# Optimization experiments

Measured on AMD Instinct MI355X. Metric: run time of the kernel, lower is better.

The kernel has to match this reference:

```python
import jax, jax.numpy as jnp
import numpy as np

B, T, D_MODEL, N_HEADS, N_KV = 2, 2048, 1024, 16, 4
HEAD = D_MODEL // N_HEADS  # 64
NEG_INF = -1e9


def sine_table(features, length):
    # standard RoPE frequency table: theta_i = 10000^(2i/d)
    fraction = jnp.arange(0, features, 2, dtype=jnp.float32) / features
    timescale = 10000.0 ** fraction  # (features/2,)
    sinusoid = jnp.arange(length, dtype=jnp.float32)[:, None] / timescale[None, :]
    sinusoid = jnp.concatenate([sinusoid, sinusoid], axis=-1)  # (L, features)
    return jnp.sin(sinusoid), jnp.cos(sinusoid)


def rotate_half(x):
    x1, x2 = jnp.split(x, 2, axis=-1)
    return jnp.concatenate([-x2, x1], axis=-1)


def apply_rope(x, sin, cos):
    # x: (B, H, T, D); sin/cos: (L, D)
    t = x.shape[-2]
    return x * cos[:t][None, None] + rotate_half(x) * sin[:t][None, None]


def setup_inputs() -> dict:
    key = jax.random.key(0)
    k1, k2, k3, k4 = jax.random.split(key, 4)
    return {
        'q': jax.random.normal(k1, (B, T, D_MODEL), dtype=jnp.float32),
        'k': jax.random.normal(k2, (B, T, N_KV * HEAD), dtype=jnp.float32),
        'v': jax.random.normal(k3, (B, T, N_KV * HEAD), dtype=jnp.float32),
        'w_out': jax.random.normal(k4, (D_MODEL, D_MODEL), dtype=jnp.float32) * 0.02,
    }


def reference(q, k, v, w_out):
    Bq, Tq, C = q.shape
    head = C // N_HEADS
    # split heads: q -> (B, n_heads, T, head); k/v -> (B, n_kv, T, head)
    qh = q.reshape(Bq, Tq, N_HEADS, head).transpose(0, 2, 1, 3)
    kh = k.reshape(Bq, Tq, N_KV, head).transpose(0, 2, 1, 3)
    vh = v.reshape(Bq, Tq, N_KV, head).transpose(0, 2, 1, 3)
    # inline RoPE on q and k
    sin, cos = sine_table(head, Tq)
    qh = apply_rope(qh, sin, cos)
    kh = apply_rope(kh, sin, cos)
    # GQA repeat of kv heads to match q heads
    rep = N_HEADS // N_KV
    kh = jnp.repeat(kh, rep, axis=1)
    vh = jnp.repeat(vh, rep, axis=1)
    # manual scaled-dot-product attention with causal masking (full T^2 logits)
    logits = jnp.einsum('bhqd,bhkd->bhqk', qh, kh) / jnp.sqrt(jnp.float32(head))
    causal = jnp.tril(jnp.ones((Tq, Tq), dtype=jnp.float32))
    logits = jnp.where(causal == 0, NEG_INF, logits)
    attn = jax.nn.softmax(logits, axis=-1)
    out = jnp.einsum('bhqk,bhkd->bhqd', attn, vh)
    out = out.transpose(0, 2, 1, 3).reshape(Bq, Tq, C)
    return out @ w_out
```

## Files before the change

### kernel.cpp

```cpp
#include <hip/hip_runtime.h>
#include <math.h>

#define T_SEQ 2048
#define NH    16
#define NKV   4

typedef __attribute__((ext_vector_type(8)))  _Float16 f16x8;
typedef __attribute__((ext_vector_type(4)))  _Float16 f16x4;
typedef __attribute__((ext_vector_type(2)))  __fp16   fp16x2b;
typedef __attribute__((ext_vector_type(4)))  float    f32x4;

#if __has_builtin(__builtin_amdgcn_exp2f)
#define EXP2F(x) __builtin_amdgcn_exp2f(x)
#else
#define EXP2F(x) exp2f(x)
#endif

#define QSCALE 0.18033688011112042f

#define LDS_BARRIER()                                        \
    do {                                                     \
        __builtin_amdgcn_sched_barrier(0);                   \
        asm volatile("s_waitcnt lgkmcnt(0)" ::: "memory");   \
        __builtin_amdgcn_s_barrier();                        \
        __builtin_amdgcn_sched_barrier(0);                   \
    } while (0)

__global__ __launch_bounds__(256) void prep_kernel(const float* __restrict__ k,
                                                   const float* __restrict__ v,
                                                   const float* __restrict__ w,
                                                   float2* __restrict__ tb,
                                                   _Float16* __restrict__ Kr,
                                                   _Float16* __restrict__ Vt,
                                                   _Float16* __restrict__ Wt)
{
    __shared__ _Float16 L[64 * 72];
    const int bx = blockIdx.x;
    if (bx < 256) {
        int idx = bx * 256 + threadIdx.x;
        int i = idx & 31, t = idx >> 5;
        float inv = __expf((float)i * (-9.210340371976184f / 32.0f));
        float ang = (float)t * inv;
        tb[idx] = make_float2(cosf(ang), sinf(ang));
    } else if (bx < 512) {
        int idx = (bx - 256) * 256 + threadIdx.x;
        int i   = idx & 31;
        int t   = idx >> 5;
        float inv = __expf((float)i * (-9.210340371976184f / 32.0f));
        float ang = (float)t * inv;
        float sn = sinf(ang), cs = cosf(ang);
        #pragma unroll
        for (int bk = 0; bk < 8; ++bk) {
            const float* src = k + ((size_t)(bk >> 2) * T_SEQ + t) * 256 + (bk & 3) * 64 + i;
            float x1 = src[0], x2 = src[32];
            _Float16* dst = Kr + ((size_t)bk * T_SEQ + t) * 64 + i;
            dst[0]  = (_Float16)(x1 * cs - x2 * sn);
            dst[32] = (_Float16)(x2 * cs + x1 * sn);
        }
    } else if (bx < 768) {
        const int id = bx - 512;
        const int t0 = (id & 31) * 64, bk = id >> 5;
        const int b = bk >> 2, kh = bk & 3;
        const int rr = threadIdx.x >> 2, pp = threadIdx.x & 3;
        const float* src = v + ((size_t)(b * T_SEQ + t0 + rr)) * 256 + kh * 64 + pp * 16;
        f32x4 s0 = *(const f32x4*)(src), s1 = *(const f32x4*)(src + 4);
        f32x4 s2 = *(const f32x4*)(src + 8), s3 = *(const f32x4*)(src + 12);
        _Float16* lp = &L[rr * 72 + pp * 16];
        #pragma unroll
        for (int j = 0; j < 4; ++j) { lp[j] = (_Float16)s0[j]; lp[4+j] = (_Float16)s1[j];
                                      lp[8+j] = (_Float16)s2[j]; lp[12+j] = (_Float16)s3[j]; }
        __syncthreads();
        f16x8 w0, w1;
        #pragma unroll
        for (int j = 0; j < 8; ++j) w0[j] = L[(pp * 16 + j) * 72 + rr];
        #pragma unroll
        for (int j = 0; j < 8; ++j) w1[j] = L[(pp * 16 + 8 + j) * 72 + rr];
        _Float16* dst = Vt + ((size_t)bk * 64 + rr) * T_SEQ + t0 + pp * 16;
        *(f16x8*)dst = w0; *(f16x8*)(dst + 8) = w1;
    } else {
        const int id = bx - 768;
        const int k0 = (id & 15) * 64, n0 = (id >> 4) * 64;
        const int rr = threadIdx.x >> 2, pp = threadIdx.x & 3;
        const float* src = w + (size_t)(k0 + rr) * 1024 + n0 + pp * 16;
        f32x4 s0 = *(const f32x4*)(src), s1 = *(const f32x4*)(src + 4);
        f32x4 s2 = *(const f32x4*)(src + 8), s3 = *(const f32x4*)(src + 12);
        _Float16* lp = &L[rr * 72 + pp * 16];
        #pragma unroll
        for (int j = 0; j < 4; ++j) { lp[j] = (_Float16)s0[j]; lp[4+j] = (_Float16)s1[j];
                                      lp[8+j] = (_Float16)s2[j]; lp[12+j] = (_Float16)s3[j]; }
        __syncthreads();
        f16x8 w0, w1;
        #pragma unroll
        for (int j = 0; j < 8; ++j) w0[j] = L[(pp * 16 + j) * 72 + rr];
        #pragma unroll
        for (int j = 0; j < 8; ++j) w1[j] = L[(pp * 16 + 8 + j) * 72 + rr];
        _Float16* dst = Wt + (size_t)(n0 + rr) * 1024 + k0 + pp * 16;
        *(f16x8*)dst = w0; *(f16x8*)(dst + 8) = w1;
    }
}


__global__ __launch_bounds__(256) void attn_kernel(const float* __restrict__ q,
                                                   const float2* __restrict__ tb,
                                                   const _Float16* __restrict__ Kr,
                                                   const _Float16* __restrict__ Vt,
                                                   _Float16* __restrict__ AO)
{
    __shared__ _Float16 smem[16384];

    const int wid  = threadIdx.x >> 6;
    const int lane = threadIdx.x & 63;
    const int bh = blockIdx.x & 31;
    const int pp = blockIdx.x >> 5;
    const int p  = (pp < 8) ? pp : (23 - pp);
    const int qb0 = p, qb1 = 31 - p;
    const int b = bh >> 4, h = bh & 15;
    const int kh = h >> 2;
    const int bkh = b * NKV + kh;
    const int g = lane >> 4, r = lane & 15;

    const int srow   = wid * 16 + (lane >> 3);
    const int schunk = lane & 7;
    const _Float16* kgbase = Kr + (size_t)bkh * T_SEQ * 64;
    const _Float16* vgbase = Vt + (size_t)bkh * 64 * T_SEQ;
    const int kd0 = srow * 64 + ((schunk ^ (srow & 7)) * 8);
    const int kd1 = kd0 + 8 * 64;

    f16x8 stK0, stK1, stV0, stV1;
    {
        const _Float16* kg = kgbase + (size_t)srow * 64 + schunk * 8;
        stK0 = *(const f16x8*)(kg);
        stK1 = *(const f16x8*)(kg + 8 * 64);
        const _Float16* vg = vgbase + (size_t)srow * T_SEQ + schunk * 8;
        stV0 = *(const f16x8*)(vg);
        stV1 = *(const f16x8*)(vg + 8 * T_SEQ);
    }

    f16x8 qa[2][2];
    #pragma unroll
    for (int tl = 0; tl < 2; ++tl) {
        const int t = (tl ? qb1 : qb0) * 64 + wid * 16 + r;
        const float* qs = q + ((size_t)b * T_SEQ + t) * 1024 + h * 64 + 8 * g;
        const float2* tp = tb + t * 32 + 8 * g;
        #pragma unroll
        for (int j = 0; j < 8; ++j) {
            float x0 = qs[j], x1 = qs[32 + j];
            float2 cs = tp[j];
            qa[tl][0][j] = (_Float16)((x0 * cs.x - x1 * cs.y) * QSCALE);
            qa[tl][1][j] = (_Float16)((x1 * cs.x + x0 * cs.y) * QSCALE);
        }
    }

    *(f16x8*)(&smem[kd0])        = stK0;
    *(f16x8*)(&smem[kd1])        = stK1;
    *(f16x8*)(&smem[8192 + kd0]) = stV0;
    *(f16x8*)(&smem[8192 + kd1]) = stV1;
    __syncthreads();

    f32x4 o[2][4];
    f32x4 o4[2];
    #pragma unroll
    for (int tl = 0; tl < 2; ++tl) {
        #pragma unroll
        for (int db = 0; db < 4; ++db) o[tl][db] = (f32x4){0.f,0.f,0.f,0.f};
        o4[tl] = (f32x4){0.f,0.f,0.f,0.f};
    }
    const f16x4 onesf = {(_Float16)1.f, (_Float16)1.f, (_Float16)1.f, (_Float16)1.f};
    float mrun[2] = {-INFINITY, -INFINITY};
    int cur = 0;

    for (int kvb = 0; kvb <= qb1; ++kvb) {
        const bool hasNext = (kvb < qb1);
        if (hasNext) {
            const int nb = (kvb + 1) * 64;
            const _Float16* kg = kgbase + (size_t)(nb + srow) * 64 + schunk * 8;
            stK0 = *(const f16x8*)(kg);
            stK1 = *(const f16x8*)(kg + 8 * 64);
            const _Float16* vg = vgbase + (size_t)srow * T_SEQ + nb + schunk * 8;
            stV0 = *(const f16x8*)(vg);
            stV1 = *(const f16x8*)(vg + 8 * T_SEQ);
        }
        const bool act0 = (kvb <= qb0);
        const _Float16* ks = smem + cur * 4096;
        const _Float16* vs = smem + 8192 + cur * 4096;

        f32x4 stt[2][4];
        __builtin_amdgcn_s_setprio(1);
        #pragma unroll
        for (int kt = 0; kt < 4; ++kt) {
            f16x8 ka0 = *(const f16x8*)(ks + (kt*16 + r) * 64 + ((g       ^ (r & 7)) * 8));
            f16x8 ka1 = *(const f16x8*)(ks + (kt*16 + r) * 64 + (((4 + g) ^ (r & 7)) * 8));
            f32x4 s1 = {0.f,0.f,0.f,0.f};
            s1 = __builtin_amdgcn_mfma_f32_16x16x32_f16(ka0, qa[1][0], s1, 0, 0, 0);
            s1 = __builtin_amdgcn_mfma_f32_16x16x32_f16(ka1, qa[1][1], s1, 0, 0, 0);
            stt[1][kt] = s1;
            if (act0) {
                f32x4 s0 = {0.f,0.f,0.f,0.f};
                s0 = __builtin_amdgcn_mfma_f32_16x16x32_f16(ka0, qa[0][0], s0, 0, 0, 0);
                s0 = __builtin_amdgcn_mfma_f32_16x16x32_f16(ka1, qa[0][1], s0, 0, 0, 0);
                stt[0][kt] = s0;
            }
        }
        __builtin_amdgcn_s_setprio(0);

        if (kvb == qb0) {
            #pragma unroll
            for (int kt = 0; kt < 4; ++kt)
                #pragma unroll
                for (int j = 0; j < 4; ++j)
                    if (kt*16 + 4*g + j > wid*16 + r) stt[0][kt][j] = -1e9f;
        }
        if (kvb == qb1) {
            #pragma unroll
            for (int kt = 0; kt < 4; ++kt)
                #pragma unroll
                for (int j = 0; j < 4; ++j)
                    if (kt*16 + 4*g + j > wid*16 + r) stt[1][kt][j] = -1e9f;
        }

        f16x4 pf[2][4];
        #pragma unroll
        for (int tl = 0; tl < 2; ++tl) {
            if (tl == 0 && !act0) continue;
            float a0 = fmaxf(fmaxf(stt[tl][0][0], stt[tl][0][1]),
                             fmaxf(stt[tl][0][2], stt[tl][0][3]));
            float a1 = fmaxf(fmaxf(stt[tl][1][0], stt[tl][1][1]),
                             fmaxf(stt[tl][1][2], stt[tl][1][3]));
            float a2 = fmaxf(fmaxf(stt[tl][2][0], stt[tl][2][1]),
                             fmaxf(stt[tl][2][2], stt[tl][2][3]));
            float a3 = fmaxf(fmaxf(stt[tl][3][0], stt[tl][3][1]),
                             fmaxf(stt[tl][3][2], stt[tl][3][3]));
            float pmL = fmaxf(fmaxf(a0, a1), fmaxf(a2, a3));
            if (!__all(pmL <= mrun[tl] + 8.0f)) {
                float pm = fmaxf(pmL, __shfl_xor(pmL, 16));
                pm = fmaxf(pm, __shfl_xor(pm, 32));
                float mn   = fmaxf(mrun[tl], pm);
                float corr = EXP2F(mrun[tl] - mn);
                mrun[tl]   = mn;
                f32x4 cf = { __shfl(corr, 4*g + 0), __shfl(corr, 4*g + 1),
                             __shfl(corr, 4*g + 2), __shfl(corr, 4*g + 3) };
                o[tl][0] *= cf; o[tl][1] *= cf; o[tl][2] *= cf; o[tl][3] *= cf;
                o4[tl]   *= cf;
            }
            #pragma unroll
            for (int kt = 0; kt < 4; ++kt) {
                float p0 = EXP2F(stt[tl][kt][0] - mrun[tl]);
                float p1 = EXP2F(stt[tl][kt][1] - mrun[tl]);
                float p2 = EXP2F(stt[tl][kt][2] - mrun[tl]);
                float p3 = EXP2F(stt[tl][kt][3] - mrun[tl]);
                union { unsigned u[2]; f16x4 v; } pk;
                union { fp16x2b hh; unsigned u; } c0, c1;
                c0.hh = __builtin_amdgcn_cvt_pkrtz(p0, p1);
                c1.hh = __builtin_amdgcn_cvt_pkrtz(p2, p3);
                pk.u[0] = c0.u; pk.u[1] = c1.u;
                pf[tl][kt] = pk.v;
            }
        }

        __builtin_amdgcn_s_setprio(1);
        #pragma unroll
        for (int kt = 0; kt < 4; ++kt) {
            const int vc = ((2*kt + (g >> 1)) ^ (r & 7)) * 8 + (g & 1) * 4;
            f16x4 v0 = *(const f16x4*)(vs + (0*16 + r) * 64 + vc);
            f16x4 v1 = *(const f16x4*)(vs + (1*16 + r) * 64 + vc);
            f16x4 v2 = *(const f16x4*)(vs + (2*16 + r) * 64 + vc);
            f16x4 v3 = *(const f16x4*)(vs + (3*16 + r) * 64 + vc);
            o[1][0] = __builtin_amdgcn_mfma_f32_16x16x16f16(pf[1][kt], v0, o[1][0], 0, 0, 0);
            o[1][1] = __builtin_amdgcn_mfma_f32_16x16x16f16(pf[1][kt], v1, o[1][1], 0, 0, 0);
            o[1][2] = __builtin_amdgcn_mfma_f32_16x16x16f16(pf[1][kt], v2, o[1][2], 0, 0, 0);
            o[1][3] = __builtin_amdgcn_mfma_f32_16x16x16f16(pf[1][kt], v3, o[1][3], 0, 0, 0);
            o4[1]   = __builtin_amdgcn_mfma_f32_16x16x16f16(pf[1][kt], onesf, o4[1], 0, 0, 0);
            if (act0) {
                o[0][0] = __builtin_amdgcn_mfma_f32_16x16x16f16(pf[0][kt], v0, o[0][0], 0, 0, 0);
                o[0][1] = __builtin_amdgcn_mfma_f32_16x16x16f16(pf[0][kt], v1, o[0][1], 0, 0, 0);
                o[0][2] = __builtin_amdgcn_mfma_f32_16x16x16f16(pf[0][kt], v2, o[0][2], 0, 0, 0);
                o[0][3] = __builtin_amdgcn_mfma_f32_16x16x16f16(pf[0][kt], v3, o[0][3], 0, 0, 0);
                o4[0]   = __builtin_amdgcn_mfma_f32_16x16x16f16(pf[0][kt], onesf, o4[0], 0, 0, 0);
            }
        }
        __builtin_amdgcn_s_setprio(0);

        if (hasNext) {
            _Float16* kw = smem + (cur ^ 1) * 4096;
            _Float16* vw = smem + 8192 + (cur ^ 1) * 4096;
            *(f16x8*)(&kw[kd0]) = stK0;
            *(f16x8*)(&kw[kd1]) = stK1;
            *(f16x8*)(&vw[kd0]) = stV0;
            *(f16x8*)(&vw[kd1]) = stV1;
            cur ^= 1;
        }
        __syncthreads();
    }

    #pragma unroll
    for (int tl = 0; tl < 2; ++tl) {
        f32x4 li;
        #pragma unroll
        for (int j = 0; j < 4; ++j) li[j] = 1.0f / o4[tl][j];
        _Float16* Os = smem + tl * 4608;
        #pragma unroll
        for (int db = 0; db < 4; ++db) {
            f32x4 ov = o[tl][db] * li;
            #pragma unroll
            for (int j = 0; j < 4; ++j)
                Os[(wid*16 + 4*g + j) * 72 + db*16 + r] = (_Float16)ov[j];
        }
    }
    __syncthreads();
    {
        const int row = threadIdx.x >> 2, part = threadIdx.x & 3;
        #pragma unroll
        for (int tl = 0; tl < 2; ++tl) {
            const int qb = tl ? qb1 : qb0;
            const _Float16* src = smem + tl * 4608 + row * 72 + part * 16;
            _Float16* dst = AO + ((size_t)b * T_SEQ + qb * 64 + row) * 1024 + h * 64 + part * 16;
            *(f16x8*)dst       = *(const f16x8*)src;
            *(f16x8*)(dst + 8) = *(const f16x8*)(src + 8);
        }
    }
}


#define AST 40
__global__ __launch_bounds__(256) void gemm_kernel(const _Float16* __restrict__ A,
                                                   const _Float16* __restrict__ Bt,
                                                   float* __restrict__ C)
{
    __shared__ _Float16 As[2][128 * AST];
    __shared__ _Float16 Bs[2][64 * AST];
    const int tid  = threadIdx.x;
    const int by   = blockIdx.x & 31;
    const int bx   = blockIdx.x >> 5;
    const int lane = tid & 63;
    const int wid  = tid >> 6;
    const int g = lane >> 4, r = lane & 15;
    const int wm = wid >> 1, wn = wid & 1;

    f32x4 acc[4][2];
    #pragma unroll
    for (int i = 0; i < 4; ++i)
        #pragma unroll
        for (int j = 0; j < 2; ++j) acc[i][j] = (f32x4){0.f,0.f,0.f,0.f};

    const int c0 = tid, c1 = tid + 256;
    const size_t a0off = (size_t)(by*128 + (c0 >> 2)) * 1024 + (c0 & 3) * 8;
    const size_t a1off = (size_t)(by*128 + (c1 >> 2)) * 1024 + (c1 & 3) * 8;
    const size_t b0off = (size_t)(bx*64  + (c0 >> 2)) * 1024 + (c0 & 3) * 8;
    const int ad0 = (c0 >> 2) * AST + (c0 & 3) * 8;
    const int ad1 = (c1 >> 2) * AST + (c1 & 3) * 8;

    f16x8 pA0 = *(const f16x8*)(A  + a0off);
    f16x8 pA1 = *(const f16x8*)(A  + a1off);
    f16x8 pB0 = *(const f16x8*)(Bt + b0off);
    *(f16x8*)(&As[0][ad0]) = pA0;
    *(f16x8*)(&As[0][ad1]) = pA1;
    *(f16x8*)(&Bs[0][ad0]) = pB0;
    f16x8 sA0B = *(const f16x8*)(A  + a0off + 32);
    f16x8 sA1B = *(const f16x8*)(A  + a1off + 32);
    f16x8 sB0B = *(const f16x8*)(Bt + b0off + 32);
    f16x8 sA0A, sA1A, sB0A;
    __syncthreads();

    auto iter_body = [&](int kt,
                         f16x8& iA0, f16x8& iA1, f16x8& iB0,
                         f16x8& oA0, f16x8& oA1, f16x8& oB0) {
        if (kt + 2 < 32) {
            iA0 = *(const f16x8*)(A  + a0off + (kt + 2) * 32);
            iA1 = *(const f16x8*)(A  + a1off + (kt + 2) * 32);
            iB0 = *(const f16x8*)(Bt + b0off + (kt + 2) * 32);
        }
        const int cur = kt & 1;
        f16x8 af[4], bfv[2];
        #pragma unroll
        for (int mi = 0; mi < 4; ++mi)
            af[mi] = *(const f16x8*)(&As[cur][(wm*64 + mi*16 + r) * AST + 8 * g]);
        #pragma unroll
        for (int ni = 0; ni < 2; ++ni)
            bfv[ni] = *(const f16x8*)(&Bs[cur][(wn*32 + ni*16 + r) * AST + 8 * g]);
        __builtin_amdgcn_s_setprio(1);
        #pragma unroll
        for (int mi = 0; mi < 4; ++mi)
            #pragma unroll
            for (int ni = 0; ni < 2; ++ni)
                acc[mi][ni] = __builtin_amdgcn_mfma_f32_16x16x32_f16(
                                  af[mi], bfv[ni], acc[mi][ni], 0, 0, 0);
        __builtin_amdgcn_s_setprio(0);
        if (kt + 1 < 32) {
            *(f16x8*)(&As[cur ^ 1][ad0]) = oA0;
            *(f16x8*)(&As[cur ^ 1][ad1]) = oA1;
            *(f16x8*)(&Bs[cur ^ 1][ad0]) = oB0;
        }
        LDS_BARRIER();
    };

    #pragma unroll 2
    for (int kt = 0; kt < 32; kt += 2) {
        iter_body(kt,     sA0A, sA1A, sB0A, sA0B, sA1B, sB0B);
        iter_body(kt + 1, sA0B, sA1B, sB0B, sA0A, sA1A, sB0A);
    }

    #pragma unroll
    for (int mi = 0; mi < 4; ++mi)
        #pragma unroll
        for (int ni = 0; ni < 2; ++ni)
            #pragma unroll
            for (int j = 0; j < 4; ++j)
                C[(size_t)(by*128 + wm*64 + mi*16 + 4*g + j) * 1024
                  + bx*64 + wn*32 + ni*16 + r] = acc[mi][ni][j];
}


extern "C" void kernel_launch(void* const* d_in, const int* in_sizes, int n_in,
                              void* d_out, int out_size, void* d_ws, size_t ws_size,
                              hipStream_t stream) {
    const float* q = (const float*)d_in[0];
    const float* k = (const float*)d_in[1];
    const float* v = (const float*)d_in[2];
    const float* w = (const float*)d_in[3];
    float* out = (float*)d_out;

    char* ws = (char*)d_ws;
    float2*   tb = (float2*)(ws);
    _Float16* Kr = (_Float16*)(ws + ((size_t)1 << 20));
    _Float16* Vt = (_Float16*)(ws + ((size_t)3 << 20));
    _Float16* Wt = (_Float16*)(ws + ((size_t)5 << 20));
    _Float16* AO = (_Float16*)(ws + ((size_t)7 << 20));

    hipLaunchKernelGGL(prep_kernel,  dim3(1024), dim3(256), 0, stream, k, v, w, tb, Kr, Vt, Wt);
    hipLaunchKernelGGL(attn_kernel,  dim3(512),  dim3(256), 0, stream, q, tb, Kr, Vt, AO);
    hipLaunchKernelGGL(gemm_kernel,  dim3(512),  dim3(256), 0, stream, AO, Wt, out);
}
```

Baseline: 72.59 us.

## Split attention KV range across two blocks and merge partial results

Each (batch, head, query-pair) attention work item is split into two halves over the KV range, doubling the grid to 1024 blocks. Each half stores its fp16 partial output plus per-row running max and denominator. A new merge kernel rescales and combines the two partials. The aim is better occupancy and load balance across the MI355X CUs. The cost is an extra kernel launch, extra global traffic for partial outputs, and another fp16 rounding step.

```diff
diff --git a/kernel.cpp b/kernel.cpp
--- a/kernel.cpp
+++ b/kernel.cpp
@@ -100,20 +100,28 @@
 }
 
 
-__global__ __launch_bounds__(256) void attn_kernel(const float* __restrict__ q,
-                                                   const float2* __restrict__ tb,
-                                                   const _Float16* __restrict__ Kr,
-                                                   const _Float16* __restrict__ Vt,
-                                                   _Float16* __restrict__ AO)
+__global__ __launch_bounds__(256, 4) void attn_kernel(const float* __restrict__ q,
+                                                      const float2* __restrict__ tb,
+                                                      const _Float16* __restrict__ Kr,
+                                                      const _Float16* __restrict__ Vt,
+                                                      _Float16* __restrict__ AO,
+                                                      _Float16* __restrict__ Op1,
+                                                      float2* __restrict__ st0,
+                                                      float2* __restrict__ st1)
 {
     __shared__ _Float16 smem[16384];
 
     const int wid  = threadIdx.x >> 6;
     const int lane = threadIdx.x & 63;
-    const int bh = blockIdx.x & 31;
-    const int pp = blockIdx.x >> 5;
-    const int p  = (pp < 8) ? pp : (23 - pp);
+    const int bid  = blockIdx.x;
+    const int bh   = bid & 31;
+    const int p    = (bid >> 5) & 15;
+    const int half = bid >> 9;
     const int qb0 = p, qb1 = 31 - p;
+    const int NTf = 32 - p;
+    const int H0  = (p <= 7) ? (16 - p) : 8;
+    const int kv_lo = half ? H0 : 0;
+    const int kv_hi = half ? NTf : H0;
     const int b = bh >> 4, h = bh & 15;
     const int kh = h >> 2;
     const int bkh = b * NKV + kh;
@@ -128,10 +136,10 @@
 
     f16x8 stK0, stK1, stV0, stV1;
     {
-        const _Float16* kg = kgbase + (size_t)srow * 64 + schunk * 8;
+        const _Float16* kg = kgbase + (size_t)(kv_lo * 64 + srow) * 64 + schunk * 8;
         stK0 = *(const f16x8*)(kg);
         stK1 = *(const f16x8*)(kg + 8 * 64);
-        const _Float16* vg = vgbase + (size_t)srow * T_SEQ + schunk * 8;
+        const _Float16* vg = vgbase + (size_t)srow * T_SEQ + kv_lo * 64 + schunk * 8;
         stV0 = *(const f16x8*)(vg);
         stV1 = *(const f16x8*)(vg + 8 * T_SEQ);
     }
@@ -169,8 +177,8 @@
     float mrun[2] = {-INFINITY, -INFINITY};
     int cur = 0;
 
-    for (int kvb = 0; kvb <= qb1; ++kvb) {
-        const bool hasNext = (kvb < qb1);
+    for (int kvb = kv_lo; kvb < kv_hi; ++kvb) {
+        const bool hasNext = (kvb + 1 < kv_hi);
         if (hasNext) {
             const int nb = (kvb + 1) * 64;
             const _Float16* kg = kgbase + (size_t)(nb + srow) * 64 + schunk * 8;
@@ -292,11 +300,27 @@
         __syncthreads();
     }
 
+    {
+        float2* st = half ? st1 : st0;
+        #pragma unroll
+        for (int tl = 0; tl < 2; ++tl) {
+            const int qb = tl ? qb1 : qb0;
+            float mr[4];
+            #pragma unroll
+            for (int j = 0; j < 4; ++j) mr[j] = __shfl(mrun[tl], 4*g + j);
+            if (r == 0) {
+                #pragma unroll
+                for (int j = 0; j < 4; ++j)
+                    st[(size_t)bh * 2048 + qb * 64 + wid * 16 + 4 * g + j] =
+                        make_float2(mr[j], o4[tl][j]);
+            }
+        }
+    }
     #pragma unroll
     for (int tl = 0; tl < 2; ++tl) {
         f32x4 li;
         #pragma unroll
-        for (int j = 0; j < 4; ++j) li[j] = 1.0f / o4[tl][j];
+        for (int j = 0; j < 4; ++j) li[j] = (o4[tl][j] > 0.f) ? (1.0f / o4[tl][j]) : 0.f;
         _Float16* Os = smem + tl * 4608;
         #pragma unroll
         for (int db = 0; db < 4; ++db) {
@@ -308,18 +332,43 @@
     }
     __syncthreads();
     {
+        _Float16* dstbase = half ? Op1 : AO;
         const int row = threadIdx.x >> 2, part = threadIdx.x & 3;
         #pragma unroll
         for (int tl = 0; tl < 2; ++tl) {
             const int qb = tl ? qb1 : qb0;
             const _Float16* src = smem + tl * 4608 + row * 72 + part * 16;
-            _Float16* dst = AO + ((size_t)b * T_SEQ + qb * 64 + row) * 1024 + h * 64 + part * 16;
+            _Float16* dst = dstbase + ((size_t)b * T_SEQ + qb * 64 + row) * 1024 + h * 64 + part * 16;
             *(f16x8*)dst       = *(const f16x8*)src;
             *(f16x8*)(dst + 8) = *(const f16x8*)(src + 8);
         }
     }
 }
 
+__global__ __launch_bounds__(256) void merge_kernel(const float2* __restrict__ st0,
+                                                    const float2* __restrict__ st1,
+                                                    const _Float16* __restrict__ Op1,
+                                                    _Float16* __restrict__ AO)
+{
+    const int gid = blockIdx.x * 256 + threadIdx.x;
+    const int r64 = gid >> 3;
+    const int h = r64 & 15, bt = r64 >> 4;
+    const size_t sidx = ((size_t)(bt >> 11) * 16 + h) * 2048 + (bt & 2047);
+    float2 s1 = st0[sidx], s2 = st1[sidx];
+    float m  = fmaxf(s1.x, s2.x);
+    float e1 = exp2f(s1.x - m) * s1.y;
+    float e2 = exp2f(s2.x - m) * s2.y;
+    float dn = 1.0f / (e1 + e2);
+    float w1 = e1 * dn, w2 = e2 * dn;
+    const size_t off = (size_t)gid * 8;
+    f16x8 o1 = *(const f16x8*)(AO + off);
+    f16x8 o2 = *(const f16x8*)(Op1 + off);
+    f16x8 om;
+    #pragma unroll
+    for (int j = 0; j < 8; ++j)
+        om[j] = (_Float16)(w1 * (float)o1[j] + w2 * (float)o2[j]);
+    *(f16x8*)(AO + off) = om;
+}
 
 #define AST 40
 __global__ __launch_bounds__(256) void gemm_kernel(const _Float16* __restrict__ A,
@@ -420,13 +469,18 @@
     float* out = (float*)d_out;
 
     char* ws = (char*)d_ws;
-    float2*   tb = (float2*)(ws);
-    _Float16* Kr = (_Float16*)(ws + ((size_t)1 << 20));
-    _Float16* Vt = (_Float16*)(ws + ((size_t)3 << 20));
-    _Float16* Wt = (_Float16*)(ws + ((size_t)5 << 20));
-    _Float16* AO = (_Float16*)(ws + ((size_t)7 << 20));
+    float2*   tb  = (float2*)(ws);
+    _Float16* Kr  = (_Float16*)(ws + ((size_t)1  << 20));
+    _Float16* Vt  = (_Float16*)(ws + ((size_t)3  << 20));
+    _Float16* Wt  = (_Float16*)(ws + ((size_t)5  << 20));
+    _Float16* AO  = (_Float16*)(ws + ((size_t)7  << 20));
+    _Float16* Op1 = (_Float16*)(ws + ((size_t)15 << 20));
+    float2*   st0 = (float2*)  (ws + ((size_t)23 << 20));
+    float2*   st1 = (float2*)  (ws + ((size_t)23 << 20) + ((size_t)1 << 19));
 
     hipLaunchKernelGGL(prep_kernel,  dim3(1024), dim3(256), 0, stream, k, v, w, tb, Kr, Vt, Wt);
-    hipLaunchKernelGGL(attn_kernel,  dim3(512),  dim3(256), 0, stream, q, tb, Kr, Vt, AO);
+    hipLaunchKernelGGL(attn_kernel,  dim3(1024), dim3(256), 0, stream, q, tb, Kr, Vt,
+                       AO, Op1, st0, st1);
+    hipLaunchKernelGGL(merge_kernel, dim3(2048), dim3(256), 0, stream, st0, st1, Op1, AO);
     hipLaunchKernelGGL(gemm_kernel,  dim3(512),  dim3(256), 0, stream, AO, Wt, out);
 }
```

Result: slower. 113.2 us (+55.9%).

## Process KV tiles in pairs with double-buffered LDS and deeper prefetch

Applied to the files above, without the earlier changes.

Restructures the attention KV loop to handle two 64-key tiles per iteration. It doubles LDS to 64KB for two buffer sets and keeps prefetches two tiles ahead in registers, so there is one barrier per pair instead of one per tile. The aim is to halve synchronization overhead and hide more global load latency. In exchange it uses more LDS and registers, which can lower occupancy, and it needs an odd-tile tail path.

```diff
diff --git a/kernel.cpp b/kernel.cpp
--- a/kernel.cpp
+++ b/kernel.cpp
@@ -106,7 +106,7 @@
                                                    const _Float16* __restrict__ Vt,
                                                    _Float16* __restrict__ AO)
 {
-    __shared__ _Float16 smem[16384];
+    __shared__ _Float16 smem[32768];
 
     const int wid  = threadIdx.x >> 6;
     const int lane = threadIdx.x & 63;
@@ -118,6 +118,8 @@
     const int kh = h >> 2;
     const int bkh = b * NKV + kh;
     const int g = lane >> 4, r = lane & 15;
+    const int NT = qb1 + 1;
+    const int npair = NT >> 1;
 
     const int srow   = wid * 16 + (lane >> 3);
     const int schunk = lane & 7;
@@ -126,14 +128,18 @@
     const int kd0 = srow * 64 + ((schunk ^ (srow & 7)) * 8);
     const int kd1 = kd0 + 8 * 64;
 
-    f16x8 stK0, stK1, stV0, stV1;
+    f16x8 sKa0, sKa1, sVa0, sVa1, sKb0, sKb1, sVb0, sVb1;
     {
         const _Float16* kg = kgbase + (size_t)srow * 64 + schunk * 8;
-        stK0 = *(const f16x8*)(kg);
-        stK1 = *(const f16x8*)(kg + 8 * 64);
+        sKa0 = *(const f16x8*)(kg);
+        sKa1 = *(const f16x8*)(kg + 8 * 64);
+        sKb0 = *(const f16x8*)(kg + 4096);
+        sKb1 = *(const f16x8*)(kg + 4096 + 8 * 64);
         const _Float16* vg = vgbase + (size_t)srow * T_SEQ + schunk * 8;
-        stV0 = *(const f16x8*)(vg);
-        stV1 = *(const f16x8*)(vg + 8 * T_SEQ);
+        sVa0 = *(const f16x8*)(vg);
+        sVa1 = *(const f16x8*)(vg + 8 * T_SEQ);
+        sVb0 = *(const f16x8*)(vg + 64);
+        sVb1 = *(const f16x8*)(vg + 8 * T_SEQ + 64);
     }
 
     f16x8 qa[2][2];
@@ -151,11 +157,25 @@
         }
     }
 
-    *(f16x8*)(&smem[kd0])        = stK0;
-    *(f16x8*)(&smem[kd1])        = stK1;
-    *(f16x8*)(&smem[8192 + kd0]) = stV0;
-    *(f16x8*)(&smem[8192 + kd1]) = stV1;
-    __syncthreads();
+    {
+        _Float16* kw = smem;
+        _Float16* vw = smem + 8192;
+        *(f16x8*)(&kw[kd0]) = sKa0;        *(f16x8*)(&kw[kd1]) = sKa1;
+        *(f16x8*)(&kw[4096 + kd0]) = sKb0; *(f16x8*)(&kw[4096 + kd1]) = sKb1;
+        *(f16x8*)(&vw[kd0]) = sVa0;        *(f16x8*)(&vw[kd1]) = sVa1;
+        *(f16x8*)(&vw[4096 + kd0]) = sVb0; *(f16x8*)(&vw[4096 + kd1]) = sVb1;
+        const _Float16* kg = kgbase + (size_t)(128 + srow) * 64 + schunk * 8;
+        sKa0 = *(const f16x8*)(kg);
+        sKa1 = *(const f16x8*)(kg + 8 * 64);
+        sKb0 = *(const f16x8*)(kg + 4096);
+        sKb1 = *(const f16x8*)(kg + 4096 + 8 * 64);
+        const _Float16* vg = vgbase + (size_t)srow * T_SEQ + 128 + schunk * 8;
+        sVa0 = *(const f16x8*)(vg);
+        sVa1 = *(const f16x8*)(vg + 8 * T_SEQ);
+        sVb0 = *(const f16x8*)(vg + 64);
+        sVb1 = *(const f16x8*)(vg + 8 * T_SEQ + 64);
+    }
+    LDS_BARRIER();
 
     f32x4 o[2][4];
     f32x4 o4[2];
@@ -167,23 +187,9 @@
     }
     const f16x4 onesf = {(_Float16)1.f, (_Float16)1.f, (_Float16)1.f, (_Float16)1.f};
     float mrun[2] = {-INFINITY, -INFINITY};
-    int cur = 0;
-
-    for (int kvb = 0; kvb <= qb1; ++kvb) {
-        const bool hasNext = (kvb < qb1);
-        if (hasNext) {
-            const int nb = (kvb + 1) * 64;
-            const _Float16* kg = kgbase + (size_t)(nb + srow) * 64 + schunk * 8;
-            stK0 = *(const f16x8*)(kg);
-            stK1 = *(const f16x8*)(kg + 8 * 64);
-            const _Float16* vg = vgbase + (size_t)srow * T_SEQ + nb + schunk * 8;
-            stV0 = *(const f16x8*)(vg);
-            stV1 = *(const f16x8*)(vg + 8 * T_SEQ);
-        }
+
+    auto tile_body = [&](int kvb, const _Float16* ks, const _Float16* vs) {
         const bool act0 = (kvb <= qb0);
-        const _Float16* ks = smem + cur * 4096;
-        const _Float16* vs = smem + 8192 + cur * 4096;
-
         f32x4 stt[2][4];
         __builtin_amdgcn_s_setprio(1);
         #pragma unroll
@@ -279,19 +285,50 @@
             }
         }
         __builtin_amdgcn_s_setprio(0);
-
-        if (hasNext) {
-            _Float16* kw = smem + (cur ^ 1) * 4096;
-            _Float16* vw = smem + 8192 + (cur ^ 1) * 4096;
-            *(f16x8*)(&kw[kd0]) = stK0;
-            *(f16x8*)(&kw[kd1]) = stK1;
-            *(f16x8*)(&vw[kd0]) = stV0;
-            *(f16x8*)(&vw[kd1]) = stV1;
-            cur ^= 1;
-        }
-        __syncthreads();
-    }
-
+    };
+
+    for (int j = 0; j < npair; ++j) {
+        const _Float16* kbuf = smem + (j & 1) * 16384;
+        const _Float16* vbuf = kbuf + 8192;
+        tile_body(2*j,     kbuf,        vbuf);
+        tile_body(2*j + 1, kbuf + 4096, vbuf + 4096);
+
+        const int t2 = 2*j + 2, t3 = 2*j + 3;
+        _Float16* kw = smem + ((j + 1) & 1) * 16384;
+        _Float16* vw = kw + 8192;
+        if (t2 < NT) {
+            *(f16x8*)(&kw[kd0]) = sKa0; *(f16x8*)(&kw[kd1]) = sKa1;
+            *(f16x8*)(&vw[kd0]) = sVa0; *(f16x8*)(&vw[kd1]) = sVa1;
+        }
+        if (t3 < NT) {
+            *(f16x8*)(&kw[4096 + kd0]) = sKb0; *(f16x8*)(&kw[4096 + kd1]) = sKb1;
+            *(f16x8*)(&vw[4096 + kd0]) = sVb0; *(f16x8*)(&vw[4096 + kd1]) = sVb1;
+        }
+        const int t4 = 2*j + 4, t5 = 2*j + 5;
+        if (t4 < NT) {
+            const _Float16* kg = kgbase + (size_t)(t4 * 64 + srow) * 64 + schunk * 8;
+            sKa0 = *(const f16x8*)(kg);
+            sKa1 = *(const f16x8*)(kg + 8 * 64);
+            const _Float16* vg = vgbase + (size_t)srow * T_SEQ + t4 * 64 + schunk * 8;
+            sVa0 = *(const f16x8*)(vg);
+            sVa1 = *(const f16x8*)(vg + 8 * T_SEQ);
+        }
+        if (t5 < NT) {
+            const _Float16* kg = kgbase + (size_t)(t5 * 64 + srow) * 64 + schunk * 8;
+            sKb0 = *(const f16x8*)(kg);
+            sKb1 = *(const f16x8*)(kg + 8 * 64);
+            const _Float16* vg = vgbase + (size_t)srow * T_SEQ + t5 * 64 + schunk * 8;
+            sVb0 = *(const f16x8*)(vg);
+            sVb1 = *(const f16x8*)(vg + 8 * T_SEQ);
+        }
+        LDS_BARRIER();
+    }
+    if (NT & 1) {
+        const _Float16* kbuf = smem + (npair & 1) * 16384;
+        tile_body(NT - 1, kbuf, kbuf + 8192);
+    }
+
+    __syncthreads();
     #pragma unroll
     for (int tl = 0; tl < 2; ++tl) {
         f32x4 li;
```

Measured after the change: 71.61 us. No clear change (-1.3%).
